# Kernel tuning notes

Measured on AMD Instinct MI355X. Metric: run time of the kernel, lower is better.

The kernel has to match this reference:

```python
import jax, jax.numpy as jnp
import numpy as np

FEATURE_SIZE = 10 * 64 * 64  # 40960
HIDDEN1 = 512
HIDDEN2 = 256
BATCH = 4096


def setup_inputs() -> dict:
    key = jax.random.key(0)
    ks = jax.random.split(key, 8)
    # Sparse binary-ish features emulated as dense uniform (math is identical).
    white_features = jax.random.uniform(ks[0], (BATCH, FEATURE_SIZE), dtype=jnp.float32)
    black_features = jax.random.uniform(ks[1], (BATCH, FEATURE_SIZE), dtype=jnp.float32)
    s_ft = 1.0 / np.sqrt(FEATURE_SIZE)
    s_fc1 = 1.0 / np.sqrt(HIDDEN1 * 2)
    s_fc2 = 1.0 / np.sqrt(HIDDEN2)
    ft_w = jax.random.uniform(ks[2], (HIDDEN1, FEATURE_SIZE), minval=-s_ft, maxval=s_ft, dtype=jnp.float32)
    ft_b = jax.random.uniform(ks[3], (HIDDEN1,), minval=-s_ft, maxval=s_ft, dtype=jnp.float32)
    fc1_w = jax.random.uniform(ks[4], (HIDDEN2, HIDDEN1 * 2), minval=-s_fc1, maxval=s_fc1, dtype=jnp.float32)
    fc1_b = jax.random.uniform(ks[5], (HIDDEN2,), minval=-s_fc1, maxval=s_fc1, dtype=jnp.float32)
    fc2_w = jax.random.uniform(ks[6], (1, HIDDEN2), minval=-s_fc2, maxval=s_fc2, dtype=jnp.float32)
    fc2_b = jax.random.uniform(ks[7], (1,), minval=-s_fc2, maxval=s_fc2, dtype=jnp.float32)
    return dict(white_features=white_features, black_features=black_features,
                ft_w=ft_w, ft_b=ft_b, fc1_w=fc1_w, fc1_b=fc1_b, fc2_w=fc2_w, fc2_b=fc2_b)


def reference(white_features, black_features, ft_w, ft_b, fc1_w, fc1_b, fc2_w, fc2_b):
    # Feature transform per perspective, clamped to [0, 1]
    white_ft = jnp.clip(white_features @ ft_w.T + ft_b, 0.0, 1.0)  # [B, H1]
    black_ft = jnp.clip(black_features @ ft_w.T + ft_b, 0.0, 1.0)  # [B, H1]
    combined = jnp.concatenate([white_ft, black_ft], axis=1)       # [B, 2*H1]
    x = jax.nn.relu(combined @ fc1_w.T + fc1_b)                    # [B, H2]
    x = x @ fc2_w.T + fc2_b                                        # [B, 1]
    return x.squeeze(-1)
```

## Files before the change

### kernel.cpp

```cpp
#include <hip/hip_runtime.h>
#include <stdint.h>

#define BATCH 4096
#define FEAT  40960
#define H1    512
#define H2    256

typedef float f32x4 __attribute__((ext_vector_type(4)));
typedef short s16x8 __attribute__((ext_vector_type(8)));
typedef unsigned int u32x2 __attribute__((ext_vector_type(2)));
typedef unsigned int u32x4 __attribute__((ext_vector_type(4)));

__device__ __forceinline__ unsigned bfpack2(float lo, float hi) {
  unsigned a = __float_as_uint(lo);
  unsigned b = __float_as_uint(hi);
  a += 0x7FFFu + ((a >> 16) & 1u);
  b += 0x7FFFu + ((b >> 16) & 1u);
  return (a >> 16) | (b & 0xFFFF0000u);
}

__device__ __forceinline__ int lds_off(int r, int kb) {
  return ((r ^ ((r >> 2) & 1)) << 6) + (kb ^ ((r & 3) << 4));
}

__device__ __forceinline__ void pipe_barrier() {
  asm volatile("s_waitcnt lgkmcnt(0)" ::: "memory");
  __builtin_amdgcn_sched_barrier(0);
  __builtin_amdgcn_s_barrier();
  __builtin_amdgcn_sched_barrier(0);
}

__global__ __launch_bounds__(512, 2)
void ft_gemm_kernel(const float* __restrict__ whiteF,
                    const float* __restrict__ blackF,
                    const float* __restrict__ ftw,
                    float* __restrict__ Ppart, int KS) {
  __shared__ char smem[81920];

  const int tid = threadIdx.x;
  const int bid = blockIdx.x;
  const int ks  = bid >> 6;
  const int p   = bid & 1;
  const int mt  = (bid >> 1) & 31;

  const float* Ag = (p == 0 ? whiteF : blackF) + (size_t)(mt * 128) * FEAT;
  const int kchunk = FEAT / KS;
  const int k0     = ks * kchunk;
  const int nsteps = kchunk >> 5;

  const int a_row = tid >> 2, a_kq = tid & 3;
  const int w_row = tid >> 3, w_kq = tid & 7;

  const float* aptr = Ag  + (size_t)a_row * FEAT + k0 + a_kq * 8;
  const float* wptr = ftw + (size_t)w_row * FEAT + k0 + w_kq * 4;

  f32x4 ra0, ra1, rw[8];
  auto issue = [&](int t) {
    const float* ap = aptr + t * 32;
    ra0 = *(const f32x4*)ap;
    ra1 = *(const f32x4*)(ap + 4);
    const float* wp = wptr + t * 32;
#pragma unroll
    for (int s = 0; s < 8; ++s)
      rw[s] = *(const f32x4*)(wp + (size_t)s * 64 * FEAT);
  };

  const int aoff_w = lds_off(a_row, a_kq * 16);
  int woff_w[8];
#pragma unroll
  for (int s = 0; s < 8; ++s)
    woff_w[s] = 8192 + lds_off(s * 64 + w_row, w_kq * 8);

  auto cvtwrite = [&](int b) {
    char* base = smem + b * 40960;
    u32x4 av;
    av.x = bfpack2(ra0.x, ra0.y); av.y = bfpack2(ra0.z, ra0.w);
    av.z = bfpack2(ra1.x, ra1.y); av.w = bfpack2(ra1.z, ra1.w);
    *(u32x4*)(base + aoff_w) = av;
#pragma unroll
    for (int s = 0; s < 8; ++s) {
      u32x2 wv;
      wv.x = bfpack2(rw[s].x, rw[s].y);
      wv.y = bfpack2(rw[s].z, rw[s].w);
      *(u32x2*)(base + woff_w[s]) = wv;
    }
  };

  const int lane = tid & 63, wave = tid >> 6;
  const int wm = wave >> 2, wn = wave & 3;
  const int lrow = lane & 15, lkb = (lane >> 4) * 16;

  int a_off[4], b_off[8];
#pragma unroll
  for (int m = 0; m < 4; ++m) a_off[m] = lds_off(wm * 64 + m * 16 + lrow, lkb);
#pragma unroll
  for (int n = 0; n < 8; ++n) b_off[n] = 8192 + lds_off(wn * 128 + n * 16 + lrow, lkb);

  f32x4 acc[4][8];
#pragma unroll
  for (int m = 0; m < 4; ++m)
#pragma unroll
    for (int n = 0; n < 8; ++n) acc[m][n] = (f32x4){0.f, 0.f, 0.f, 0.f};

  issue(0);
  for (int t = 0; t < nsteps; ++t) {
    const int b = t & 1;
    cvtwrite(b);
    if (t + 1 < nsteps) issue(t + 1);
    pipe_barrier();
    char* base = smem + b * 40960;
    s16x8 af[4];
#pragma unroll
    for (int m = 0; m < 4; ++m) af[m] = *(const s16x8*)(base + a_off[m]);
#pragma unroll
    for (int n = 0; n < 8; ++n) {
      s16x8 bfn = *(const s16x8*)(base + b_off[n]);
#pragma unroll
      for (int m = 0; m < 4; ++m)
        acc[m][n] = __builtin_amdgcn_mfma_f32_16x16x32_bf16(af[m], bfn, acc[m][n], 0, 0, 0);
    }
  }

  float* Pp = Ppart + ((size_t)(ks * 2 + p) * BATCH + mt * 128) * H1;
  const int r0 = wm * 64 + (lane >> 4) * 4;
  const int c0 = wn * 128 + lrow;
#pragma unroll
  for (int m = 0; m < 4; ++m)
#pragma unroll
    for (int n = 0; n < 8; ++n) {
      float* dst = Pp + (size_t)(r0 + m * 16) * H1 + c0 + n * 16;
#pragma unroll
      for (int j = 0; j < 4; ++j) dst[(size_t)j * H1] = acc[m][n][j];
    }
}

__global__ __launch_bounds__(256)
void ft_reduce_kernel(const float* __restrict__ Ppart,
                      const float* __restrict__ ftb,
                      unsigned short* __restrict__ comb, int KS) {
  const size_t gid = (size_t)blockIdx.x * 256 + threadIdx.x;
  const int    pp  = (int)(gid / (BATCH * H1 / 4));
  const size_t rem = gid % (BATCH * H1 / 4);
  const int    row = (int)(rem / (H1 / 4));
  const int    n4  = (int)(rem % (H1 / 4)) * 4;

  f32x4 s = (f32x4){0.f, 0.f, 0.f, 0.f};
  for (int ks = 0; ks < KS; ++ks)
    s += *(const f32x4*)(Ppart + ((size_t)(ks * 2 + pp) * BATCH + row) * H1 + n4);
  const f32x4 bv = *(const f32x4*)(ftb + n4);
  s += bv;
  s.x = fminf(fmaxf(s.x, 0.f), 1.f);
  s.y = fminf(fmaxf(s.y, 0.f), 1.f);
  s.z = fminf(fmaxf(s.z, 0.f), 1.f);
  s.w = fminf(fmaxf(s.w, 0.f), 1.f);

  u32x2 o;
  o.x = bfpack2(s.x, s.y);
  o.y = bfpack2(s.z, s.w);
  *(u32x2*)(comb + (size_t)row * 1024 + pp * H1 + n4) = o;
}

__global__ __launch_bounds__(256)
void fc_kernel(const unsigned short* __restrict__ comb,
               const float* __restrict__ w1, const float* __restrict__ b1,
               const float* __restrict__ w2, const float* __restrict__ b2,
               float* __restrict__ out) {
  __shared__ char smem[40960];
  __shared__ float rowsum[64];

  const int tid = threadIdx.x;
  const int bm  = blockIdx.x;
  if (tid < 64) rowsum[tid] = 0.f;

  const int a_row = tid >> 2, a_kq = tid & 3;
  const unsigned short* aptr = comb + (size_t)(bm * 64 + a_row) * 1024 + a_kq * 8;
  const float* wptr = w1 + (size_t)a_row * 1024 + a_kq * 8;

  u32x4 raA;
  f32x4 rw0[4], rw1[4];
  auto issue = [&](int t) {
    raA = *(const u32x4*)(aptr + t * 32);
    const float* wp = wptr + t * 32;
#pragma unroll
    for (int s = 0; s < 4; ++s) {
      rw0[s] = *(const f32x4*)(wp + (size_t)s * 64 * 1024);
      rw1[s] = *(const f32x4*)(wp + (size_t)s * 64 * 1024 + 4);
    }
  };

  const int aoff_w = lds_off(a_row, a_kq * 16);
  int woff_w[4];
#pragma unroll
  for (int s = 0; s < 4; ++s)
    woff_w[s] = 4096 + lds_off(s * 64 + a_row, a_kq * 16);

  auto cvtwrite = [&](int b) {
    char* base = smem + b * 20480;
    *(u32x4*)(base + aoff_w) = raA;
#pragma unroll
    for (int s = 0; s < 4; ++s) {
      u32x4 wv;
      wv.x = bfpack2(rw0[s].x, rw0[s].y); wv.y = bfpack2(rw0[s].z, rw0[s].w);
      wv.z = bfpack2(rw1[s].x, rw1[s].y); wv.w = bfpack2(rw1[s].z, rw1[s].w);
      *(u32x4*)(base + woff_w[s]) = wv;
    }
  };

  const int lane = tid & 63, wn = tid >> 6;
  const int lrow = lane & 15, lkb = (lane >> 4) * 16;
  int a_off[4], b_off[4];
#pragma unroll
  for (int m = 0; m < 4; ++m) a_off[m] = lds_off(m * 16 + lrow, lkb);
#pragma unroll
  for (int n = 0; n < 4; ++n) b_off[n] = 4096 + lds_off(wn * 64 + n * 16 + lrow, lkb);

  f32x4 acc[4][4];
#pragma unroll
  for (int m = 0; m < 4; ++m)
#pragma unroll
    for (int n = 0; n < 4; ++n) acc[m][n] = (f32x4){0.f, 0.f, 0.f, 0.f};

  issue(0);
  for (int t = 0; t < 32; ++t) {
    const int b = t & 1;
    cvtwrite(b);
    if (t + 1 < 32) issue(t + 1);
    pipe_barrier();
    char* base = smem + b * 20480;
    s16x8 af[4];
#pragma unroll
    for (int m = 0; m < 4; ++m) af[m] = *(const s16x8*)(base + a_off[m]);
#pragma unroll
    for (int n = 0; n < 4; ++n) {
      s16x8 bfn = *(const s16x8*)(base + b_off[n]);
#pragma unroll
      for (int m = 0; m < 4; ++m)
        acc[m][n] = __builtin_amdgcn_mfma_f32_16x16x32_bf16(af[m], bfn, acc[m][n], 0, 0, 0);
    }
  }

  float b1v[4], w2v[4];
#pragma unroll
  for (int n = 0; n < 4; ++n) {
    const int col = wn * 64 + n * 16 + lrow;
    b1v[n] = b1[col];
    w2v[n] = w2[col];
  }
#pragma unroll
  for (int m = 0; m < 4; ++m)
#pragma unroll
    for (int j = 0; j < 4; ++j) {
      float v = 0.f;
#pragma unroll
      for (int n = 0; n < 4; ++n) {
        float x = acc[m][n][j] + b1v[n];
        x = fmaxf(x, 0.f);
        v += x * w2v[n];
      }
#pragma unroll
      for (int d = 1; d < 16; d <<= 1) v += __shfl_xor(v, d, 64);
      if ((lane & 15) == 0)
        atomicAdd(&rowsum[m * 16 + (lane >> 4) * 4 + j], v);
    }
  __syncthreads();
  if (tid < 64) {
    out[bm * 64 + tid] = rowsum[tid] + b2[0];
  }
}

extern "C" void kernel_launch(void* const* d_in, const int* in_sizes, int n_in,
                              void* d_out, int out_size, void* d_ws, size_t ws_size,
                              hipStream_t stream) {
  const float* whiteF = (const float*)d_in[0];
  const float* blackF = (const float*)d_in[1];
  const float* ftw    = (const float*)d_in[2];
  const float* ftb    = (const float*)d_in[3];
  const float* w1     = (const float*)d_in[4];
  const float* b1     = (const float*)d_in[5];
  const float* w2     = (const float*)d_in[6];
  const float* b2     = (const float*)d_in[7];

  const size_t per_split  = (size_t)2 * BATCH * H1 * sizeof(float);
  const size_t comb_bytes = (size_t)BATCH * 1024 * sizeof(unsigned short);
  int KS = 8;
  while (KS > 1 && (size_t)KS * per_split + comb_bytes > ws_size) KS >>= 1;

  float* Ppart = (float*)d_ws;
  unsigned short* comb = (unsigned short*)((char*)d_ws + (size_t)KS * per_split);
  float* outp = (float*)d_out;

  hipLaunchKernelGGL(ft_gemm_kernel, dim3(64 * KS), dim3(512), 0, stream,
                     whiteF, blackF, ftw, Ppart, KS);
  hipLaunchKernelGGL(ft_reduce_kernel, dim3((2 * BATCH * H1 / 4) / 256), dim3(256),
                     0, stream, Ppart, ftb, comb, KS);
  hipLaunchKernelGGL(fc_kernel, dim3(BATCH / 64), dim3(256), 0, stream,
                     comb, w1, b1, w2, b2, outp);
}
```

Before: 669.8 us.

## Pre-convert FT weights to swizzled bf16 tiles and stream via global_load_lds

```diff
diff --git a/kernel.cpp b/kernel.cpp
--- a/kernel.cpp
+++ b/kernel.cpp
@@ -4,7 +4,11 @@
 #define BATCH 4096
 #define FEAT  40960
 #define H1    512
-#define H2    256
+#define KS    4
+#define KCHUNK (FEAT / KS)
+#define NSTEPS (KCHUNK / 32)
+#define NTILES (FEAT / 32)
+#define WTILE  32768
 
 typedef float f32x4 __attribute__((ext_vector_type(4)));
 typedef short s16x8 __attribute__((ext_vector_type(8)));
@@ -19,82 +23,61 @@
   return (a >> 16) | (b & 0xFFFF0000u);
 }
 
-__device__ __forceinline__ int lds_off(int r, int kb) {
-  return ((r ^ ((r >> 2) & 1)) << 6) + (kb ^ ((r & 3) << 4));
-}
-
-__device__ __forceinline__ void pipe_barrier() {
-  asm volatile("s_waitcnt lgkmcnt(0)" ::: "memory");
-  __builtin_amdgcn_sched_barrier(0);
-  __builtin_amdgcn_s_barrier();
-  __builtin_amdgcn_sched_barrier(0);
+__device__ __forceinline__ int lds_swz(int r, int cb) {
+  return (r << 6) + (cb ^ (((r >> 1) & 3) << 4));
+}
+
+__device__ __forceinline__ void glds16(const void* g, void* l) {
+  __builtin_amdgcn_global_load_lds(
+      (const __attribute__((address_space(1))) unsigned*)g,
+      (__attribute__((address_space(3))) unsigned*)l, 16, 0, 0);
+}
+
+__global__ __launch_bounds__(512)
+void wcvt_kernel(const float* __restrict__ ftw, char* __restrict__ wbf) {
+  const int bid = blockIdx.x;
+  const int T = bid >> 2, rq = bid & 3;
+  const int tid = threadIdx.x;
+  const int r = rq * 128 + (tid >> 2), kq = tid & 3;
+  const float* src = ftw + (size_t)r * FEAT + T * 32 + kq * 8;
+  f32x4 v0 = *(const f32x4*)src;
+  f32x4 v1 = *(const f32x4*)(src + 4);
+  u32x4 o;
+  o.x = bfpack2(v0.x, v0.y); o.y = bfpack2(v0.z, v0.w);
+  o.z = bfpack2(v1.x, v1.y); o.w = bfpack2(v1.z, v1.w);
+  *(u32x4*)(wbf + (size_t)T * WTILE + lds_swz(r, kq * 16)) = o;
 }
 
 __global__ __launch_bounds__(512, 2)
 void ft_gemm_kernel(const float* __restrict__ whiteF,
                     const float* __restrict__ blackF,
-                    const float* __restrict__ ftw,
-                    float* __restrict__ Ppart, int KS) {
+                    const char* __restrict__ wbf,
+                    float* __restrict__ Ppart) {
   __shared__ char smem[81920];
 
-  const int tid = threadIdx.x;
-  const int bid = blockIdx.x;
-  const int ks  = bid >> 6;
-  const int p   = bid & 1;
-  const int mt  = (bid >> 1) & 31;
-
-  const float* Ag = (p == 0 ? whiteF : blackF) + (size_t)(mt * 128) * FEAT;
-  const int kchunk = FEAT / KS;
-  const int k0     = ks * kchunk;
-  const int nsteps = kchunk >> 5;
+  const int tid = threadIdx.x, bid = blockIdx.x;
+  const int ks = bid >> 6;
+  const int p  = bid & 1;
+  const int mt = (bid >> 1) & 31;
+
+  const float* Ag =
+      (p == 0 ? whiteF : blackF) + (size_t)(mt * 128) * FEAT + ks * KCHUNK;
 
   const int a_row = tid >> 2, a_kq = tid & 3;
-  const int w_row = tid >> 3, w_kq = tid & 7;
-
-  const float* aptr = Ag  + (size_t)a_row * FEAT + k0 + a_kq * 8;
-  const float* wptr = ftw + (size_t)w_row * FEAT + k0 + w_kq * 4;
-
-  f32x4 ra0, ra1, rw[8];
-  auto issue = [&](int t) {
-    const float* ap = aptr + t * 32;
-    ra0 = *(const f32x4*)ap;
-    ra1 = *(const f32x4*)(ap + 4);
-    const float* wp = wptr + t * 32;
-#pragma unroll
-    for (int s = 0; s < 8; ++s)
-      rw[s] = *(const f32x4*)(wp + (size_t)s * 64 * FEAT);
-  };
-
-  const int aoff_w = lds_off(a_row, a_kq * 16);
-  int woff_w[8];
-#pragma unroll
-  for (int s = 0; s < 8; ++s)
-    woff_w[s] = 8192 + lds_off(s * 64 + w_row, w_kq * 8);
-
-  auto cvtwrite = [&](int b) {
-    char* base = smem + b * 40960;
-    u32x4 av;
-    av.x = bfpack2(ra0.x, ra0.y); av.y = bfpack2(ra0.z, ra0.w);
-    av.z = bfpack2(ra1.x, ra1.y); av.w = bfpack2(ra1.z, ra1.w);
-    *(u32x4*)(base + aoff_w) = av;
-#pragma unroll
-    for (int s = 0; s < 8; ++s) {
-      u32x2 wv;
-      wv.x = bfpack2(rw[s].x, rw[s].y);
-      wv.y = bfpack2(rw[s].z, rw[s].w);
-      *(u32x2*)(base + woff_w[s]) = wv;
-    }
-  };
+  const float* aptr = Ag + (size_t)a_row * FEAT + a_kq * 8;
+  const int awoff = lds_swz(a_row, a_kq * 16);
 
   const int lane = tid & 63, wave = tid >> 6;
+  const char* wsrc = wbf + (size_t)(ks * NSTEPS) * WTILE + wave * 4096 + lane * 16;
+  const int wdst = 8192 + wave * 4096;
+
   const int wm = wave >> 2, wn = wave & 3;
   const int lrow = lane & 15, lkb = (lane >> 4) * 16;
-
   int a_off[4], b_off[8];
 #pragma unroll
-  for (int m = 0; m < 4; ++m) a_off[m] = lds_off(wm * 64 + m * 16 + lrow, lkb);
-#pragma unroll
-  for (int n = 0; n < 8; ++n) b_off[n] = 8192 + lds_off(wn * 128 + n * 16 + lrow, lkb);
+  for (int m = 0; m < 4; ++m) a_off[m] = lds_swz(wm * 64 + m * 16 + lrow, lkb);
+#pragma unroll
+  for (int n = 0; n < 8; ++n) b_off[n] = 8192 + lds_swz(wn * 128 + n * 16 + lrow, lkb);
 
   f32x4 acc[4][8];
 #pragma unroll
@@ -102,24 +85,56 @@
 #pragma unroll
     for (int n = 0; n < 8; ++n) acc[m][n] = (f32x4){0.f, 0.f, 0.f, 0.f};
 
-  issue(0);
-  for (int t = 0; t < nsteps; ++t) {
-    const int b = t & 1;
-    cvtwrite(b);
-    if (t + 1 < nsteps) issue(t + 1);
-    pipe_barrier();
-    char* base = smem + b * 40960;
-    s16x8 af[4];
-#pragma unroll
-    for (int m = 0; m < 4; ++m) af[m] = *(const s16x8*)(base + a_off[m]);
-#pragma unroll
-    for (int n = 0; n < 8; ++n) {
-      s16x8 bfn = *(const s16x8*)(base + b_off[n]);
-#pragma unroll
-      for (int m = 0; m < 4; ++m)
-        acc[m][n] = __builtin_amdgcn_mfma_f32_16x16x32_bf16(af[m], bfn, acc[m][n], 0, 0, 0);
-    }
-  }
+  f32x4 raA[2], raB[2];
+
+#pragma unroll
+  for (int c = 0; c < 4; ++c) glds16(wsrc + c * 1024, smem + wdst + c * 1024);
+  raA[0] = *(const f32x4*)aptr;
+  raB[0] = *(const f32x4*)(aptr + 4);
+
+#define GSTEP(B, LAST, t)                                                     \
+  {                                                                           \
+    if (!(LAST)) {                                                            \
+      const float* ap = aptr + (size_t)((t) + 1) * 32;                        \
+      raA[(B) ^ 1] = *(const f32x4*)ap;                                       \
+      raB[(B) ^ 1] = *(const f32x4*)(ap + 4);                                 \
+    }                                                                         \
+    u32x4 av;                                                                 \
+    av.x = bfpack2(raA[B].x, raA[B].y); av.y = bfpack2(raA[B].z, raA[B].w);   \
+    av.z = bfpack2(raB[B].x, raB[B].y); av.w = bfpack2(raB[B].z, raB[B].w);   \
+    *(u32x4*)(smem + (B) * 40960 + awoff) = av;                               \
+    __builtin_amdgcn_sched_barrier(0);                                        \
+    if (LAST) { asm volatile("s_waitcnt vmcnt(0) lgkmcnt(0)" ::: "memory"); } \
+    else      { asm volatile("s_waitcnt vmcnt(2) lgkmcnt(0)" ::: "memory"); } \
+    __builtin_amdgcn_sched_barrier(0);                                        \
+    __builtin_amdgcn_s_barrier();                                             \
+    __builtin_amdgcn_sched_barrier(0);                                        \
+    const char* base = smem + (B) * 40960;                                    \
+    s16x8 af[4];                                                              \
+    _Pragma("unroll") for (int m = 0; m < 4; ++m)                             \
+        af[m] = *(const s16x8*)(base + a_off[m]);                             \
+    s16x8 bfr[8];                                                             \
+    _Pragma("unroll") for (int n = 0; n < 8; ++n)                             \
+        bfr[n] = *(const s16x8*)(base + b_off[n]);                            \
+    if (!(LAST)) {                                                            \
+      const char* wsp = wsrc + (size_t)((t) + 1) * WTILE;                     \
+      char* wdp = smem + ((B) ^ 1) * 40960 + wdst;                            \
+      _Pragma("unroll") for (int c = 0; c < 4; ++c)                           \
+          glds16(wsp + c * 1024, wdp + c * 1024);                             \
+    }                                                                         \
+    _Pragma("unroll") for (int n = 0; n < 8; ++n)                             \
+      _Pragma("unroll") for (int m = 0; m < 4; ++m)                           \
+          acc[m][n] = __builtin_amdgcn_mfma_f32_16x16x32_bf16(                \
+              af[m], bfr[n], acc[m][n], 0, 0, 0);                             \
+  }
+
+  for (int tt = 0; tt < NSTEPS - 2; tt += 2) {
+    GSTEP(0, false, tt);
+    GSTEP(1, false, tt + 1);
+  }
+  GSTEP(0, false, NSTEPS - 2);
+  GSTEP(1, true, NSTEPS - 1);
+#undef GSTEP
 
   float* Pp = Ppart + ((size_t)(ks * 2 + p) * BATCH + mt * 128) * H1;
   const int r0 = wm * 64 + (lane >> 4) * 4;
@@ -137,7 +152,7 @@
 __global__ __launch_bounds__(256)
 void ft_reduce_kernel(const float* __restrict__ Ppart,
                       const float* __restrict__ ftb,
-                      unsigned short* __restrict__ comb, int KS) {
+                      unsigned short* __restrict__ comb) {
   const size_t gid = (size_t)blockIdx.x * 256 + threadIdx.x;
   const int    pp  = (int)(gid / (BATCH * H1 / 4));
   const size_t rem = gid % (BATCH * H1 / 4);
@@ -145,6 +160,7 @@
   const int    n4  = (int)(rem % (H1 / 4)) * 4;
 
   f32x4 s = (f32x4){0.f, 0.f, 0.f, 0.f};
+#pragma unroll
   for (int ks = 0; ks < KS; ++ks)
     s += *(const f32x4*)(Ppart + ((size_t)(ks * 2 + pp) * BATCH + row) * H1 + n4);
   const f32x4 bv = *(const f32x4*)(ftb + n4);
@@ -188,11 +204,11 @@
     }
   };
 
-  const int aoff_w = lds_off(a_row, a_kq * 16);
+  const int aoff_w = lds_swz(a_row, a_kq * 16);
   int woff_w[4];
 #pragma unroll
   for (int s = 0; s < 4; ++s)
-    woff_w[s] = 4096 + lds_off(s * 64 + a_row, a_kq * 16);
+    woff_w[s] = 4096 + lds_swz(s * 64 + a_row, a_kq * 16);
 
   auto cvtwrite = [&](int b) {
     char* base = smem + b * 20480;
@@ -210,9 +226,9 @@
   const int lrow = lane & 15, lkb = (lane >> 4) * 16;
   int a_off[4], b_off[4];
 #pragma unroll
-  for (int m = 0; m < 4; ++m) a_off[m] = lds_off(m * 16 + lrow, lkb);
-#pragma unroll
-  for (int n = 0; n < 4; ++n) b_off[n] = 4096 + lds_off(wn * 64 + n * 16 + lrow, lkb);
+  for (int m = 0; m < 4; ++m) a_off[m] = lds_swz(m * 16 + lrow, lkb);
+#pragma unroll
+  for (int n = 0; n < 4; ++n) b_off[n] = 4096 + lds_swz(wn * 64 + n * 16 + lrow, lkb);
 
   f32x4 acc[4][4];
 #pragma unroll
@@ -225,7 +241,10 @@
     const int b = t & 1;
     cvtwrite(b);
     if (t + 1 < 32) issue(t + 1);
-    pipe_barrier();
+    asm volatile("s_waitcnt lgkmcnt(0)" ::: "memory");
+    __builtin_amdgcn_sched_barrier(0);
+    __builtin_amdgcn_s_barrier();
+    __builtin_amdgcn_sched_barrier(0);
     char* base = smem + b * 20480;
     s16x8 af[4];
 #pragma unroll
@@ -280,19 +299,18 @@
   const float* w2     = (const float*)d_in[6];
   const float* b2     = (const float*)d_in[7];
 
-  const size_t per_split  = (size_t)2 * BATCH * H1 * sizeof(float);
-  const size_t comb_bytes = (size_t)BATCH * 1024 * sizeof(unsigned short);
-  int KS = 8;
-  while (KS > 1 && (size_t)KS * per_split + comb_bytes > ws_size) KS >>= 1;
-
-  float* Ppart = (float*)d_ws;
-  unsigned short* comb = (unsigned short*)((char*)d_ws + (size_t)KS * per_split);
+  char* wbf = (char*)d_ws;
+  const size_t wbf_bytes   = (size_t)NTILES * WTILE;
+  const size_t ppart_bytes = (size_t)KS * 2 * BATCH * H1 * sizeof(float);
+  float* Ppart = (float*)((char*)d_ws + wbf_bytes);
+  unsigned short* comb = (unsigned short*)((char*)d_ws + wbf_bytes + ppart_bytes);
   float* outp = (float*)d_out;
 
+  hipLaunchKernelGGL(wcvt_kernel, dim3(NTILES * 4), dim3(512), 0, stream, ftw, wbf);
   hipLaunchKernelGGL(ft_gemm_kernel, dim3(64 * KS), dim3(512), 0, stream,
-                     whiteF, blackF, ftw, Ppart, KS);
+                     whiteF, blackF, wbf, Ppart);
   hipLaunchKernelGGL(ft_reduce_kernel, dim3((2 * BATCH * H1 / 4) / 256), dim3(256),
-                     0, stream, Ppart, ftb, comb, KS);
+                     0, stream, Ppart, ftb, comb);
   hipLaunchKernelGGL(fc_kernel, dim3(BATCH / 64), dim3(256), 0, stream,
                      comb, w1, b1, w2, b2, outp);
 }
```

Result: faster. 584.6 us (-12.7%).
